# Kernel optimization log

Hardware: AMD Instinct MI355X
Metric: run time of the kernel (lower is better)

Reference implementation:

```python
import jax, jax.numpy as jnp
import numpy as np
from jax import lax

B, C, H, W = 2, 256, 64, 64
OUT_C = 256
D_QK = C // 16   # 16
D_V = C // 2     # 128
BN_EPS = 1e-5


def setup_inputs() -> dict:
    key = jax.random.key(0)
    ks = jax.random.split(key, 10)
    s = lambda fan: 1.0 / np.sqrt(fan)
    return {
        "input1": jax.random.normal(ks[0], (B, C, H, W), jnp.float32),
        "input2": jax.random.normal(ks[1], (B, C, H, W), jnp.float32),
        "Wq": jax.random.normal(ks[2], (D_QK, C), jnp.float32) * s(C),
        "bq": jnp.zeros((D_QK,), jnp.float32),
        "Wk": jax.random.normal(ks[3], (D_QK, C), jnp.float32) * s(C),
        "bk": jnp.zeros((D_QK,), jnp.float32),
        "Wv": jax.random.normal(ks[4], (D_V, C), jnp.float32) * s(C),
        "bv": jnp.zeros((D_V,), jnp.float32),
        "gamma": jnp.array(0.5, jnp.float32),  # nn.Parameter(zeros(1)); nonzero to exercise the path
        "Wcat": jax.random.normal(ks[5], (OUT_C, C, 3, 3), jnp.float32) * s(C * 9),
        "bn_gamma": jnp.ones((OUT_C,), jnp.float32),
        "bn_beta": jnp.zeros((OUT_C,), jnp.float32),
    }


def _conv1x1(x, Wt, b):
    # x: (B,C,H,W), Wt: (O,C) -> (B,O,H,W)
    return jnp.einsum('bchw,oc->bohw', x, Wt) + b[None, :, None, None]


def _branch(x_self, x_other, Wq, bq, Wk, bk, Wv, bv, gamma):
    N = H * W
    q = _conv1x1(x_self, Wq, bq).reshape(B, D_QK, N)   # q of self
    k = _conv1x1(x_other, Wk, bk).reshape(B, D_QK, N)  # k of other
    v = _conv1x1(x_self, Wv, bv).reshape(B, D_V, N)    # v of self
    # attn[b,n,m] = softmax_m( q[:,n] . k[:,m] / sqrt(d) )
    attn = jax.nn.softmax(jnp.einsum('bdn,bdm->bnm', q, k) / jnp.sqrt(jnp.float32(D_QK)), axis=-1)
    out = jnp.einsum('bcm,bnm->bcn', v, attn).reshape(B, D_V, H, W)  # v @ attn^T
    out = jnp.concatenate([out, x_self[:, :C // 2]], axis=1)  # (B,C,H,W)
    return gamma * out + x_self


def reference(input1, input2, Wq, bq, Wk, bk, Wv, bv, gamma, Wcat, bn_gamma, bn_beta):
    out1 = _branch(input1, input2, Wq, bq, Wk, bk, Wv, bv, gamma)
    out2 = _branch(input2, input1, Wq, bq, Wk, bk, Wv, bv, gamma)
    s = out1 + out2
    y = lax.conv_general_dilated(s, Wcat, (1, 1), 'SAME',
                                 dimension_numbers=('NCHW', 'OIHW', 'NCHW'))
    # BatchNorm (inference: running_mean=0, running_var=1)
    inv = 1.0 / jnp.sqrt(1.0 + BN_EPS)
    y = y * (bn_gamma * inv)[None, :, None, None] + bn_beta[None, :, None, None]
    feat_sum = jax.nn.relu(y)
    return (feat_sum, out1, out2)
```

## Files before the change

kernel.cpp:

```cpp
#include <hip/hip_runtime.h>

#define N_PIX 4096
#define CCH 256
#define DV 128

typedef __attribute__((ext_vector_type(8))) short bf16x8;
typedef __attribute__((ext_vector_type(4))) float f32x4;
typedef __attribute__((ext_vector_type(8))) short short8;

__device__ __forceinline__ short f2bf(float f) {
    unsigned u = __builtin_bit_cast(unsigned, f);
    u += 0x7fffu + ((u >> 16) & 1u);
    return (short)(u >> 16);
}

__device__ __forceinline__ float4 bf4_load(const short* p) {
    short4 s = *(const short4*)p;
    float4 f;
    f.x = __builtin_bit_cast(float, (unsigned)((unsigned short)s.x) << 16);
    f.y = __builtin_bit_cast(float, (unsigned)((unsigned short)s.y) << 16);
    f.z = __builtin_bit_cast(float, (unsigned)((unsigned short)s.z) << 16);
    f.w = __builtin_bit_cast(float, (unsigned)((unsigned short)s.w) << 16);
    return f;
}

__global__ __launch_bounds__(512) void qkv_kernel(
    const float* __restrict__ x1, const float* __restrict__ x2,
    const short* __restrict__ wqkv,
    const float* __restrict__ bq, const float* __restrict__ bk,
    const float* __restrict__ bv,
    short* __restrict__ qb, short* __restrict__ kb, short* __restrict__ vb)
{
    __shared__ short xT[64][68];

    const int tid = threadIdx.x;
    const int lane = tid & 63;
    const int w = tid >> 6;
    const int g = lane >> 4, l15 = lane & 15;
    const int n0 = blockIdx.x * 64;
    const int ib = blockIdx.y;
    const int i = ib >> 1, b = ib & 1;
    const float* x = (i == 0 ? x1 : x2) + (size_t)b * CCH * N_PIX;

    const int px2 = tid & 31, c4 = tid >> 5;
    const int rhalf = (w >> 2) * 80;

    f32x4 acc[5];
    #pragma unroll
    for (int jl = 0; jl < 5; ++jl) {
        int rbase = rhalf + jl * 16;
        float bias;
        if (rbase == 0)       bias = bq[l15];
        else if (rbase == 16) bias = bk[l15];
        else                  bias = bv[rbase - 32 + l15];
        acc[jl] = (f32x4){bias, bias, bias, bias};
    }

    float2 xr[4];
    {
        #pragma unroll
        for (int jj = 0; jj < 4; ++jj)
            xr[jj] = *(const float2*)&x[(size_t)(c4 * 4 + jj) * N_PIX + n0 + px2 * 2];
    }

    for (int ci = 0; ci < 4; ++ci) {
        __syncthreads();
        {
            short4 w0, w1;
            w0.x = f2bf(xr[0].x); w0.y = f2bf(xr[1].x); w0.z = f2bf(xr[2].x); w0.w = f2bf(xr[3].x);
            w1.x = f2bf(xr[0].y); w1.y = f2bf(xr[1].y); w1.z = f2bf(xr[2].y); w1.w = f2bf(xr[3].y);
            *(short4*)&xT[px2 * 2 + 0][c4 * 4] = w0;
            *(short4*)&xT[px2 * 2 + 1][c4 * 4] = w1;
        }
        __syncthreads();
        if (ci < 3) {
            #pragma unroll
            for (int jj = 0; jj < 4; ++jj)
                xr[jj] = *(const float2*)
                    &x[(size_t)((ci + 1) * 64 + c4 * 4 + jj) * N_PIX + n0 + px2 * 2];
        }
        bf16x8 a0 = *(const bf16x8*)&xT[(w & 3) * 16 + l15][g * 8];
        bf16x8 a1 = *(const bf16x8*)&xT[(w & 3) * 16 + l15][32 + g * 8];
        #pragma unroll
        for (int jl = 0; jl < 5; ++jl) {
            int rbase = rhalf + jl * 16;
            const short* wrow = wqkv + (size_t)(rbase + l15) * CCH + ci * 64;
            bf16x8 b0 = *(const bf16x8*)&wrow[g * 8];
            bf16x8 b1 = *(const bf16x8*)&wrow[32 + g * 8];
            acc[jl] = __builtin_amdgcn_mfma_f32_16x16x32_bf16(a0, b0, acc[jl], 0, 0, 0);
            acc[jl] = __builtin_amdgcn_mfma_f32_16x16x32_bf16(a1, b1, acc[jl], 0, 0, 0);
        }
    }

    const int px_base = n0 + (w & 3) * 16 + g * 4;
    #pragma unroll
    for (int jl = 0; jl < 5; ++jl) {
        int rbase = rhalf + jl * 16;
        if (rbase == 0) {
            #pragma unroll
            for (int rr = 0; rr < 4; ++rr)
                qb[((size_t)ib * N_PIX + px_base + rr) * 16 + l15] = f2bf(acc[jl][rr]);
        } else if (rbase == 16) {
            #pragma unroll
            for (int rr = 0; rr < 4; ++rr)
                kb[((size_t)ib * N_PIX + px_base + rr) * 16 + l15] = f2bf(acc[jl][rr]);
        } else {
            int c = rbase - 32 + l15;
            short4 s;
            s.x = f2bf(acc[jl][0]); s.y = f2bf(acc[jl][1]);
            s.z = f2bf(acc[jl][2]); s.w = f2bf(acc[jl][3]);
            *(short4*)&vb[((size_t)ib * DV + c) * N_PIX + px_base] = s;
        }
    }
}

__global__ __launch_bounds__(256, 4) void attn_kernel(
    const short* __restrict__ qg, const short* __restrict__ kg,
    const short* __restrict__ vg,
    float* __restrict__ out1, float* __restrict__ out2,
    short* __restrict__ featp, float* __restrict__ lpart)
{
    __shared__ short k_lds[64 * 24];
    __shared__ short p_lds[64 * 72];

    const int tid = threadIdx.x;
    const int lane = tid & 63;
    const int w = tid >> 6;
    const int gk = lane >> 4;
    const int l15 = lane & 15;

    const int B_ = blockIdx.x;
    const int pb = B_ & 3;
    const int mh = (B_ >> 2) % 3;
    const int nt = B_ / 12;
    const int n0 = nt * 64;
    const int br = pb >> 1, b = pb & 1;
    const int tstart = mh * 22;
    const int tend = (mh == 2) ? 64 : tstart + 22;

    const short* qp = qg + (size_t)pb * N_PIX * 16;
    const short* kp = kg + (size_t)((br ^ 1) * 2 + b) * N_PIX * 16;
    const short* vp = vg + (size_t)pb * DV * N_PIX;

    bf16x8 aq = {};
    if (lane < 32)
        aq = *(const bf16x8*)&qp[(size_t)(n0 + w * 16 + l15) * 16 + gk * 8];

    f32x4 acc[2][4];
    #pragma unroll
    for (int cc = 0; cc < 2; ++cc)
        #pragma unroll
        for (int nb = 0; nb < 4; ++nb) acc[cc][nb] = (f32x4){0.f, 0.f, 0.f, 0.f};
    float lsum[4] = {0.f, 0.f, 0.f, 0.f};

    const short* vbase = vp + (size_t)(w * 32 + l15) * N_PIX + gk * 8;
    const int krow = tid - 192;

    int4 vbuf0[4], vbuf1[4];
    int4 kr0 = {}, kr1 = {};

    {
        #pragma unroll
        for (int cc = 0; cc < 2; ++cc)
            #pragma unroll
            for (int m2 = 0; m2 < 2; ++m2)
                vbuf0[cc * 2 + m2] = *(const int4*)
                    &vbase[(size_t)cc * 16 * N_PIX + tstart * 64 + m2 * 32];
        if (tid >= 192) {
            kr0 = *(const int4*)&kp[(size_t)(tstart * 64 + krow) * 16];
            kr1 = *(const int4*)&kp[(size_t)(tstart * 64 + krow) * 16 + 8];
            *(int4*)&k_lds[krow * 24] = kr0;
            *(int4*)&k_lds[krow * 24 + 8] = kr1;
        }
        __syncthreads();
    }

    for (int t0 = tstart; t0 < tend; t0 += 2) {
        #pragma unroll
        for (int half = 0; half < 2; ++half) {
            const int t = t0 + half;
            int4* vcur = half ? vbuf1 : vbuf0;
            int4* vnxt = half ? vbuf0 : vbuf1;
            if (t + 1 < tend) {
                #pragma unroll
                for (int cc = 0; cc < 2; ++cc)
                    #pragma unroll
                    for (int m2 = 0; m2 < 2; ++m2)
                        vnxt[cc * 2 + m2] = *(const int4*)
                            &vbase[(size_t)cc * 16 * N_PIX + (t + 1) * 64 + m2 * 32];
                if (tid >= 192) {
                    kr0 = *(const int4*)&kp[(size_t)((t + 1) * 64 + krow) * 16];
                    kr1 = *(const int4*)&kp[(size_t)((t + 1) * 64 + krow) * 16 + 8];
                }
            }
            #pragma unroll
            for (int h = 0; h < 4; ++h) {
                bf16x8 bk_ = {};
                if (lane < 32)
                    bk_ = *(const bf16x8*)&k_lds[(h * 16 + l15) * 24 + gk * 8];
                f32x4 s = __builtin_amdgcn_mfma_f32_16x16x32_bf16(
                    aq, bk_, (f32x4){0.f, 0.f, 0.f, 0.f}, 0, 0, 0);
                #pragma unroll
                for (int rr = 0; rr < 4; ++rr) {
                    float e = __expf(s[rr] * 0.25f);
                    lsum[rr] += e;
                    unsigned u = __builtin_bit_cast(unsigned, e);
                    p_lds[(w * 16 + gk * 4 + rr) * 72 + h * 16 + l15] = (short)(u >> 16);
                }
            }
            __syncthreads();
            if (t + 1 < tend && tid >= 192) {
                *(int4*)&k_lds[krow * 24] = kr0;
                *(int4*)&k_lds[krow * 24 + 8] = kr1;
            }
            __builtin_amdgcn_s_setprio(1);
            #pragma unroll
            for (int m2 = 0; m2 < 2; ++m2) {
                #pragma unroll
                for (int nb = 0; nb < 4; ++nb) {
                    bf16x8 bp = *(const bf16x8*)&p_lds[(nb * 16 + l15) * 72 + m2 * 32 + gk * 8];
                    #pragma unroll
                    for (int cc = 0; cc < 2; ++cc) {
                        bf16x8 av = __builtin_bit_cast(bf16x8, vcur[cc * 2 + m2]);
                        acc[cc][nb] = __builtin_amdgcn_mfma_f32_16x16x32_bf16(
                            av, bp, acc[cc][nb], 0, 0, 0);
                    }
                }
            }
            __builtin_amdgcn_s_setprio(0);
            __syncthreads();
        }
    }

    #pragma unroll
    for (int rr = 0; rr < 4; ++rr) {
        float v = lsum[rr];
        v += __shfl_xor(v, 1); v += __shfl_xor(v, 2);
        v += __shfl_xor(v, 4); v += __shfl_xor(v, 8);
        lsum[rr] = v;
    }
    if (l15 == 0) {
        #pragma unroll
        for (int rr = 0; rr < 4; ++rr)
            lpart[(size_t)(pb * 3 + mh) * N_PIX + n0 + w * 16 + gk * 4 + rr] = lsum[rr];
    }

    if (mh == 0) {
        float* Od = (br ? out2 : out1) + (size_t)b * CCH * N_PIX;
        #pragma unroll
        for (int cc = 0; cc < 2; ++cc)
            #pragma unroll
            for (int nb = 0; nb < 4; ++nb)
                #pragma unroll
                for (int rr = 0; rr < 4; ++rr) {
                    int c = w * 32 + cc * 16 + gk * 4 + rr;
                    Od[(size_t)c * N_PIX + n0 + nb * 16 + l15] = acc[cc][nb][rr];
                }
    } else {
        short* Ps = featp + (size_t)(pb * 2 + (mh - 1)) * (64 * 128 * 64)
                          + (size_t)nt * (128 * 64);
        #pragma unroll
        for (int chalf = 0; chalf < 2; ++chalf) {
            if ((w >> 1) == chalf) {
                int crel_base = (w & 1) * 32;
                #pragma unroll
                for (int cc = 0; cc < 2; ++cc)
                    #pragma unroll
                    for (int nb = 0; nb < 4; ++nb)
                        #pragma unroll
                        for (int rr = 0; rr < 4; ++rr) {
                            int crel = crel_base + cc * 16 + gk * 4 + rr;
                            p_lds[crel * 66 + nb * 16 + l15] = f2bf(acc[cc][nb][rr]);
                        }
            }
            __syncthreads();
            for (int idx = tid; idx < 512; idx += 256) {
                int cr = idx >> 3, seg = idx & 7;
                int4 v = *(const int4*)&p_lds[cr * 66 + seg * 8];
                *(int4*)&Ps[(size_t)(chalf * 64 + cr) * 64 + seg * 8] = v;
            }
            __syncthreads();
        }
    }
}

__global__ __launch_bounds__(256) void merge_kernel(
    const float* __restrict__ x1, const float* __restrict__ x2,
    const short* __restrict__ featp, const float* __restrict__ lpart,
    const float* __restrict__ gamma_p,
    float* __restrict__ out1, float* __restrict__ out2,
    short* __restrict__ s_t)
{
    __shared__ short st[32 * 264];
    __shared__ float rls[2][32];
    const int tid = threadIdx.x;
    const int px0 = blockIdx.x * 32;
    const int b = blockIdx.y;
    const int nt = blockIdx.x >> 1;
    const int q32 = (blockIdx.x & 1) * 32;
    const float* xa_ = x1 + (size_t)b * CCH * N_PIX;
    const float* xb_ = x2 + (size_t)b * CCH * N_PIX;
    float* o1 = out1 + (size_t)b * CCH * N_PIX;
    float* o2 = out2 + (size_t)b * CCH * N_PIX;
    const short* T10 = featp + (size_t)(b * 2 + 0) * (64 * 128 * 64) + (size_t)nt * (128 * 64);
    const short* T11 = featp + (size_t)(b * 2 + 1) * (64 * 128 * 64) + (size_t)nt * (128 * 64);
    const short* T20 = featp + (size_t)((2 + b) * 2 + 0) * (64 * 128 * 64) + (size_t)nt * (128 * 64);
    const short* T21 = featp + (size_t)((2 + b) * 2 + 1) * (64 * 128 * 64) + (size_t)nt * (128 * 64);

    if (tid < 64) {
        int h = tid >> 5, j = tid & 31;
        int pbh = h ? (2 + b) : b;
        float l = lpart[(size_t)(pbh * 3 + 0) * N_PIX + px0 + j]
                + lpart[(size_t)(pbh * 3 + 1) * N_PIX + px0 + j]
                + lpart[(size_t)(pbh * 3 + 2) * N_PIX + px0 + j];
        rls[h][j] = 1.0f / l;
    }
    __syncthreads();
    const float gmm = gamma_p[0];

    for (int idx = tid; idx < 2048; idx += 256) {
        int c = idx >> 3, p4 = idx & 7;
        size_t off = (size_t)c * N_PIX + px0 + p4 * 4;
        float4 va = *(const float4*)&xa_[off];
        float4 vb2 = *(const float4*)&xb_[off];
        float4 r1, r2;
        if (c < 128) {
            int toff = c * 64 + q32 + p4 * 4;
            float4 pa = *(const float4*)&o1[off];
            float4 pc = *(const float4*)&o2[off];
            float4 a1 = bf4_load(&T10[toff]);
            float4 a2 = bf4_load(&T11[toff]);
            float4 c1 = bf4_load(&T20[toff]);
            float4 c2 = bf4_load(&T21[toff]);
            r1.x = gmm * (pa.x + a1.x + a2.x) * rls[0][p4 * 4 + 0] + va.x;
            r1.y = gmm * (pa.y + a1.y + a2.y) * rls[0][p4 * 4 + 1] + va.y;
            r1.z = gmm * (pa.z + a1.z + a2.z) * rls[0][p4 * 4 + 2] + va.z;
            r1.w = gmm * (pa.w + a1.w + a2.w) * rls[0][p4 * 4 + 3] + va.w;
            r2.x = gmm * (pc.x + c1.x + c2.x) * rls[1][p4 * 4 + 0] + vb2.x;
            r2.y = gmm * (pc.y + c1.y + c2.y) * rls[1][p4 * 4 + 1] + vb2.y;
            r2.z = gmm * (pc.z + c1.z + c2.z) * rls[1][p4 * 4 + 2] + vb2.z;
            r2.w = gmm * (pc.w + c1.w + c2.w) * rls[1][p4 * 4 + 3] + vb2.w;
        } else {
            size_t offl = (size_t)(c - 128) * N_PIX + px0 + p4 * 4;
            float4 val = *(const float4*)&xa_[offl];
            float4 vbl = *(const float4*)&xb_[offl];
            r1.x = gmm * val.x + va.x; r1.y = gmm * val.y + va.y;
            r1.z = gmm * val.z + va.z; r1.w = gmm * val.w + va.w;
            r2.x = gmm * vbl.x + vb2.x; r2.y = gmm * vbl.y + vb2.y;
            r2.z = gmm * vbl.z + vb2.z; r2.w = gmm * vbl.w + vb2.w;
        }
        *(float4*)&o1[off] = r1;
        *(float4*)&o2[off] = r2;
        st[(p4 * 4 + 0) * 264 + c] = f2bf(r1.x + r2.x);
        st[(p4 * 4 + 1) * 264 + c] = f2bf(r1.y + r2.y);
        st[(p4 * 4 + 2) * 264 + c] = f2bf(r1.z + r2.z);
        st[(p4 * 4 + 3) * 264 + c] = f2bf(r1.w + r2.w);
    }
    __syncthreads();
    for (int idx = tid; idx < 1024; idx += 256) {
        int px = idx >> 5, seg = idx & 31;
        int4 v = *(const int4*)&st[px * 264 + seg * 8];
        *(int4*)&s_t[((size_t)b * N_PIX + px0 + px) * CCH + seg * 8] = v;
    }
}

__global__ __launch_bounds__(256) void prep_w(
    const float* __restrict__ Wcat,
    const float* __restrict__ Wq, const float* __restrict__ Wk,
    const float* __restrict__ Wv,
    short* __restrict__ wfmt, short* __restrict__ wqkv)
{
    if (blockIdx.x < 288) {
        int idx = blockIdx.x * 256 + threadIdx.x;
        int lane = idx & 63;
        int ocg = (idx >> 6) & 15;
        int chunk = (idx >> 10) & 7;
        int tap = idx >> 13;
        int oc = ocg * 16 + (lane & 15);
        int ic0 = chunk * 32 + (lane >> 4) * 8;
        short8 v;
        #pragma unroll
        for (int j = 0; j < 8; ++j)
            v[j] = f2bf(Wcat[((size_t)oc * CCH + ic0 + j) * 9 + tap]);
        *(short8*)&wfmt[(size_t)idx * 8] = v;
    } else {
        int idx = (blockIdx.x - 288) * 1024 + threadIdx.x * 4;
        int r = idx >> 8, c = idx & 255;
        const float* src;
        if (r < 16)      src = Wq + (size_t)r * CCH + c;
        else if (r < 32) src = Wk + (size_t)(r - 16) * CCH + c;
        else             src = Wv + (size_t)(r - 32) * CCH + c;
        float4 f = *(const float4*)src;
        short4 s;
        s.x = f2bf(f.x); s.y = f2bf(f.y); s.z = f2bf(f.z); s.w = f2bf(f.w);
        *(short4*)&wqkv[idx] = s;
    }
}

__global__ __launch_bounds__(256, 2) void conv_mfma(
    const short* __restrict__ s_t, const short* __restrict__ wfmt,
    const float* __restrict__ bn_gamma, const float* __restrict__ bn_beta,
    float* __restrict__ feat)
{
    __shared__ short s_lds[198 * 40];
    const int tid = threadIdx.x;
    const int lane = tid & 63;
    const int wv = tid >> 6;
    const int g = lane >> 4, l15 = lane & 15;

    const int bx = blockIdx.x;
    const int oc_t = bx & 3;
    const int pt = bx >> 2;
    const int b = pt >> 6;
    const int h0 = pt & 63;

    f32x4 acc[4] = {};

    const short* sbase = s_t + (size_t)b * N_PIX * CCH;
    const short* wf = wfmt + ((size_t)(oc_t * 4) * 64 + lane) * 8;

    for (int ci = 0; ci < 8; ++ci) {
        const int ic0 = ci * 32;
        __syncthreads();
        for (int idx = tid; idx < 792; idx += 256) {
            int seg = idx & 3, pos = idx >> 2;
            int row = pos / 66, wi = pos - row * 66;
            int hr = h0 - 1 + row, w = wi - 1;
            int4 val = {0, 0, 0, 0};
            if (hr >= 0 && hr < 64 && (unsigned)w < 64u)
                val = *(const int4*)&sbase[((size_t)(hr * 64 + w)) * CCH + ic0 + seg * 8];
            *(int4*)&s_lds[pos * 40 + seg * 8] = val;
        }
        __syncthreads();

        const short* wfc = wf + (size_t)ci * 8192;
        bf16x8 a0[4], a1[4];
        #pragma unroll
        for (int j = 0; j < 4; ++j) a0[j] = *(const bf16x8*)&wfc[j * 512];

        for (int tap = 0; tap < 9; ++tap) {
            bf16x8* ac = (tap & 1) ? a1 : a0;
            bf16x8* an = (tap & 1) ? a0 : a1;
            if (tap < 8) {
                const short* wfn = wfc + (size_t)(tap + 1) * 65536;
                #pragma unroll
                for (int j = 0; j < 4; ++j) an[j] = *(const bf16x8*)&wfn[j * 512];
            }
            int ky = (tap >= 6) ? 2 : (tap >= 3 ? 1 : 0);
            int kx = tap - ky * 3;
            bf16x8 bb = *(const bf16x8*)
                &s_lds[(ky * 66 + wv * 16 + l15 + kx) * 40 + g * 8];
            #pragma unroll
            for (int j = 0; j < 4; ++j)
                acc[j] = __builtin_amdgcn_mfma_f32_16x16x32_bf16(
                    ac[j], bb, acc[j], 0, 0, 0);
        }
    }

    const float inv = rsqrtf(1.0f + 1e-5f);
    const int wcol = wv * 16 + l15;
    #pragma unroll
    for (int j = 0; j < 4; ++j) {
        #pragma unroll
        for (int r = 0; r < 4; ++r) {
            int oc = oc_t * 64 + j * 16 + g * 4 + r;
            float y = acc[j][r] * (bn_gamma[oc] * inv) + bn_beta[oc];
            feat[((size_t)b * CCH + oc) * N_PIX + h0 * 64 + wcol] = fmaxf(y, 0.f);
        }
    }
}

extern "C" void kernel_launch(void* const* d_in, const int* in_sizes, int n_in,
                              void* d_out, int out_size, void* d_ws, size_t ws_size,
                              hipStream_t stream) {
    const float* x1    = (const float*)d_in[0];
    const float* x2    = (const float*)d_in[1];
    const float* Wq    = (const float*)d_in[2];
    const float* bq    = (const float*)d_in[3];
    const float* Wk    = (const float*)d_in[4];
    const float* bk    = (const float*)d_in[5];
    const float* Wv    = (const float*)d_in[6];
    const float* bv    = (const float*)d_in[7];
    const float* gamma = (const float*)d_in[8];
    const float* Wcat  = (const float*)d_in[9];
    const float* bng   = (const float*)d_in[10];
    const float* bnb   = (const float*)d_in[11];

    float* out  = (float*)d_out;
    float* feat = out;
    float* out1 = out + 2097152;
    float* out2 = out + 4194304;

    short* ws   = (short*)d_ws;
    short* qb   = ws;
    short* kb   = ws + 262144;
    short* vb   = ws + 524288;
    short* s_t  = ws + 2621440;
    short* wfmt = ws + 4718592;
    float* lp   = (float*)(ws + 5308416);
    short* wqkv = s_t;

    prep_w<<<328, 256, 0, stream>>>(Wcat, Wq, Wk, Wv, wfmt, wqkv);
    qkv_kernel<<<dim3(64, 4), 512, 0, stream>>>(x1, x2, wqkv, bq, bk, bv, qb, kb, vb);
    attn_kernel<<<768, 256, 0, stream>>>(qb, kb, vb, out1, out2, (short*)feat, lp);
    merge_kernel<<<dim3(128, 2), 256, 0, stream>>>(x1, x2, (const short*)feat, lp, gamma, out1, out2, s_t);
    conv_mfma<<<512, 256, 0, stream>>>(s_t, wfmt, bng, bnb, feat);
}
```

Measured before the change: 107.1 us.

## Load K fragments directly to registers and double-buffer P tile to drop barrier

The attention kernel no longer stages K through shared memory. Each lane now loads its MFMA K fragments straight from global memory into double-buffered registers. The P tile in LDS is double-buffered by half-step, which removes the second __syncthreads per inner step; the LDS row pitch also changes from 72 to 68. The extra register buffers lower the launch-bounds occupancy hint from 4 to 3 blocks per CU, which may reduce latency hiding.

```diff
diff --git a/kernel.cpp b/kernel.cpp
--- a/kernel.cpp
+++ b/kernel.cpp
@@ -114,14 +114,13 @@
     }
 }
 
-__global__ __launch_bounds__(256, 4) void attn_kernel(
+__global__ __launch_bounds__(256, 3) void attn_kernel(
     const short* __restrict__ qg, const short* __restrict__ kg,
     const short* __restrict__ vg,
     float* __restrict__ out1, float* __restrict__ out2,
     short* __restrict__ featp, float* __restrict__ lpart)
 {
-    __shared__ short k_lds[64 * 24];
-    __shared__ short p_lds[64 * 72];
+    __shared__ short p_lds[2][64 * 68];
 
     const int tid = threadIdx.x;
     const int lane = tid & 63;
@@ -154,10 +153,10 @@
     float lsum[4] = {0.f, 0.f, 0.f, 0.f};
 
     const short* vbase = vp + (size_t)(w * 32 + l15) * N_PIX + gk * 8;
-    const int krow = tid - 192;
+    const short* kfrag = kp + (size_t)l15 * 16 + gk * 8;
 
     int4 vbuf0[4], vbuf1[4];
-    int4 kr0 = {}, kr1 = {};
+    int4 kbuf0[4] = {}, kbuf1[4] = {};
 
     {
         #pragma unroll
@@ -166,13 +165,11 @@
             for (int m2 = 0; m2 < 2; ++m2)
                 vbuf0[cc * 2 + m2] = *(const int4*)
                     &vbase[(size_t)cc * 16 * N_PIX + tstart * 64 + m2 * 32];
-        if (tid >= 192) {
-            kr0 = *(const int4*)&kp[(size_t)(tstart * 64 + krow) * 16];
-            kr1 = *(const int4*)&kp[(size_t)(tstart * 64 + krow) * 16 + 8];
-            *(int4*)&k_lds[krow * 24] = kr0;
-            *(int4*)&k_lds[krow * 24 + 8] = kr1;
-        }
-        __syncthreads();
+        if (lane < 32) {
+            #pragma unroll
+            for (int h = 0; h < 4; ++h)
+                kbuf0[h] = *(const int4*)&kfrag[(size_t)(tstart * 64 + h * 16) * 16];
+        }
     }
 
     for (int t0 = tstart; t0 < tend; t0 += 2) {
@@ -181,6 +178,9 @@
             const int t = t0 + half;
             int4* vcur = half ? vbuf1 : vbuf0;
             int4* vnxt = half ? vbuf0 : vbuf1;
+            int4* kcur = half ? kbuf1 : kbuf0;
+            int4* knxt = half ? kbuf0 : kbuf1;
+            short* pcur = &p_lds[half][0];
             if (t + 1 < tend) {
                 #pragma unroll
                 for (int cc = 0; cc < 2; ++cc)
@@ -188,16 +188,15 @@
                     for (int m2 = 0; m2 < 2; ++m2)
                         vnxt[cc * 2 + m2] = *(const int4*)
                             &vbase[(size_t)cc * 16 * N_PIX + (t + 1) * 64 + m2 * 32];
-                if (tid >= 192) {
-                    kr0 = *(const int4*)&kp[(size_t)((t + 1) * 64 + krow) * 16];
-                    kr1 = *(const int4*)&kp[(size_t)((t + 1) * 64 + krow) * 16 + 8];
+                if (lane < 32) {
+                    #pragma unroll
+                    for (int h = 0; h < 4; ++h)
+                        knxt[h] = *(const int4*)&kfrag[(size_t)((t + 1) * 64 + h * 16) * 16];
                 }
             }
             #pragma unroll
             for (int h = 0; h < 4; ++h) {
-                bf16x8 bk_ = {};
-                if (lane < 32)
-                    bk_ = *(const bf16x8*)&k_lds[(h * 16 + l15) * 24 + gk * 8];
+                bf16x8 bk_ = __builtin_bit_cast(bf16x8, kcur[h]);
                 f32x4 s = __builtin_amdgcn_mfma_f32_16x16x32_bf16(
                     aq, bk_, (f32x4){0.f, 0.f, 0.f, 0.f}, 0, 0, 0);
                 #pragma unroll
@@ -205,20 +204,16 @@
                     float e = __expf(s[rr] * 0.25f);
                     lsum[rr] += e;
                     unsigned u = __builtin_bit_cast(unsigned, e);
-                    p_lds[(w * 16 + gk * 4 + rr) * 72 + h * 16 + l15] = (short)(u >> 16);
+                    pcur[(w * 16 + gk * 4 + rr) * 68 + h * 16 + l15] = (short)(u >> 16);
                 }
             }
             __syncthreads();
-            if (t + 1 < tend && tid >= 192) {
-                *(int4*)&k_lds[krow * 24] = kr0;
-                *(int4*)&k_lds[krow * 24 + 8] = kr1;
-            }
             __builtin_amdgcn_s_setprio(1);
             #pragma unroll
             for (int m2 = 0; m2 < 2; ++m2) {
                 #pragma unroll
                 for (int nb = 0; nb < 4; ++nb) {
-                    bf16x8 bp = *(const bf16x8*)&p_lds[(nb * 16 + l15) * 72 + m2 * 32 + gk * 8];
+                    bf16x8 bp = *(const bf16x8*)&pcur[(nb * 16 + l15) * 68 + m2 * 32 + gk * 8];
                     #pragma unroll
                     for (int cc = 0; cc < 2; ++cc) {
                         bf16x8 av = __builtin_bit_cast(bf16x8, vcur[cc * 2 + m2]);
@@ -228,7 +223,6 @@
                 }
             }
             __builtin_amdgcn_s_setprio(0);
-            __syncthreads();
         }
     }
 
@@ -257,6 +251,8 @@
                     Od[(size_t)c * N_PIX + n0 + nb * 16 + l15] = acc[cc][nb][rr];
                 }
     } else {
+        __syncthreads();
+        short* pf = &p_lds[0][0];
         short* Ps = featp + (size_t)(pb * 2 + (mh - 1)) * (64 * 128 * 64)
                           + (size_t)nt * (128 * 64);
         #pragma unroll
@@ -270,13 +266,13 @@
                         #pragma unroll
                         for (int rr = 0; rr < 4; ++rr) {
                             int crel = crel_base + cc * 16 + gk * 4 + rr;
-                            p_lds[crel * 66 + nb * 16 + l15] = f2bf(acc[cc][nb][rr]);
+                            pf[crel * 66 + nb * 16 + l15] = f2bf(acc[cc][nb][rr]);
                         }
             }
             __syncthreads();
             for (int idx = tid; idx < 512; idx += 256) {
                 int cr = idx >> 3, seg = idx & 7;
-                int4 v = *(const int4*)&p_lds[cr * 66 + seg * 8];
+                int4 v = *(const int4*)&pf[cr * 66 + seg * 8];
                 *(int4*)&Ps[(size_t)(chalf * 64 + cr) * 64 + seg * 8] = v;
             }
             __syncthreads();
```

Result: slower. 142.1 us (+32.7%).

## Retile PV MFMA warps to 64ch x 32pix and single-buffer V loads

Applied to the files above, without the earlier changes.

Changes the per-warp output tile of the P·V product from 32 channels × 64 pixels to 64 channels × 32 pixels, so each warp reads half as many P fragments from LDS but holds twice as many V fragments. The double-buffered V register prefetch is replaced by a single buffer refilled after the MFMA block of each tile, and the unroll-by-two loop becomes a plain per-tile loop. This keeps the register count roughly the same but gives up the overlap of the V global loads with compute, so V load latency may be exposed before the next barrier.

```diff
diff --git a/kernel.cpp b/kernel.cpp
--- a/kernel.cpp
+++ b/kernel.cpp
@@ -146,25 +146,28 @@
     if (lane < 32)
         aq = *(const bf16x8*)&qp[(size_t)(n0 + w * 16 + l15) * 16 + gk * 8];
 
-    f32x4 acc[2][4];
+    const int ch = w & 1;
+    const int nh = w >> 1;
+
+    f32x4 acc[4][2];
     #pragma unroll
-    for (int cc = 0; cc < 2; ++cc)
-        #pragma unroll
-        for (int nb = 0; nb < 4; ++nb) acc[cc][nb] = (f32x4){0.f, 0.f, 0.f, 0.f};
+    for (int cc = 0; cc < 4; ++cc)
+        #pragma unroll
+        for (int nb = 0; nb < 2; ++nb) acc[cc][nb] = (f32x4){0.f, 0.f, 0.f, 0.f};
     float lsum[4] = {0.f, 0.f, 0.f, 0.f};
 
-    const short* vbase = vp + (size_t)(w * 32 + l15) * N_PIX + gk * 8;
+    const short* vbase = vp + (size_t)(ch * 64 + l15) * N_PIX + gk * 8;
     const int krow = tid - 192;
 
-    int4 vbuf0[4], vbuf1[4];
+    int4 vbuf[8];
     int4 kr0 = {}, kr1 = {};
 
     {
         #pragma unroll
-        for (int cc = 0; cc < 2; ++cc)
+        for (int cc = 0; cc < 4; ++cc)
             #pragma unroll
             for (int m2 = 0; m2 < 2; ++m2)
-                vbuf0[cc * 2 + m2] = *(const int4*)
+                vbuf[cc * 2 + m2] = *(const int4*)
                     &vbase[(size_t)cc * 16 * N_PIX + tstart * 64 + m2 * 32];
         if (tid >= 192) {
             kr0 = *(const int4*)&kp[(size_t)(tstart * 64 + krow) * 16];
@@ -175,61 +178,56 @@
         __syncthreads();
     }
 
-    for (int t0 = tstart; t0 < tend; t0 += 2) {
-        #pragma unroll
-        for (int half = 0; half < 2; ++half) {
-            const int t = t0 + half;
-            int4* vcur = half ? vbuf1 : vbuf0;
-            int4* vnxt = half ? vbuf0 : vbuf1;
-            if (t + 1 < tend) {
+    for (int t = tstart; t < tend; ++t) {
+        if (t + 1 < tend && tid >= 192) {
+            kr0 = *(const int4*)&kp[(size_t)((t + 1) * 64 + krow) * 16];
+            kr1 = *(const int4*)&kp[(size_t)((t + 1) * 64 + krow) * 16 + 8];
+        }
+        #pragma unroll
+        for (int h = 0; h < 4; ++h) {
+            bf16x8 bk_ = {};
+            if (lane < 32)
+                bk_ = *(const bf16x8*)&k_lds[(h * 16 + l15) * 24 + gk * 8];
+            f32x4 s = __builtin_amdgcn_mfma_f32_16x16x32_bf16(
+                aq, bk_, (f32x4){0.f, 0.f, 0.f, 0.f}, 0, 0, 0);
+            #pragma unroll
+            for (int rr = 0; rr < 4; ++rr) {
+                float e = __expf(s[rr] * 0.25f);
+                lsum[rr] += e;
+                unsigned u = __builtin_bit_cast(unsigned, e);
+                p_lds[(w * 16 + gk * 4 + rr) * 72 + h * 16 + l15] = (short)(u >> 16);
+            }
+        }
+        __syncthreads();
+        if (t + 1 < tend && tid >= 192) {
+            *(int4*)&k_lds[krow * 24] = kr0;
+            *(int4*)&k_lds[krow * 24 + 8] = kr1;
+        }
+        __builtin_amdgcn_s_setprio(1);
+        #pragma unroll
+        for (int m2 = 0; m2 < 2; ++m2) {
+            #pragma unroll
+            for (int nb = 0; nb < 2; ++nb) {
+                bf16x8 bp = *(const bf16x8*)
+                    &p_lds[(nh * 32 + nb * 16 + l15) * 72 + m2 * 32 + gk * 8];
                 #pragma unroll
-                for (int cc = 0; cc < 2; ++cc)
-                    #pragma unroll
-                    for (int m2 = 0; m2 < 2; ++m2)
-                        vnxt[cc * 2 + m2] = *(const int4*)
-                            &vbase[(size_t)cc * 16 * N_PIX + (t + 1) * 64 + m2 * 32];
-                if (tid >= 192) {
-                    kr0 = *(const int4*)&kp[(size_t)((t + 1) * 64 + krow) * 16];
-                    kr1 = *(const int4*)&kp[(size_t)((t + 1) * 64 + krow) * 16 + 8];
+                for (int cc = 0; cc < 4; ++cc) {
+                    bf16x8 av = __builtin_bit_cast(bf16x8, vbuf[cc * 2 + m2]);
+                    acc[cc][nb] = __builtin_amdgcn_mfma_f32_16x16x32_bf16(
+                        av, bp, acc[cc][nb], 0, 0, 0);
                 }
             }
-            #pragma unroll
-            for (int h = 0; h < 4; ++h) {
-                bf16x8 bk_ = {};
-                if (lane < 32)
-                    bk_ = *(const bf16x8*)&k_lds[(h * 16 + l15) * 24 + gk * 8];
-                f32x4 s = __builtin_amdgcn_mfma_f32_16x16x32_bf16(
-                    aq, bk_, (f32x4){0.f, 0.f, 0.f, 0.f}, 0, 0, 0);
+        }
+        __builtin_amdgcn_s_setprio(0);
+        if (t + 1 < tend) {
+            #pragma unroll
+            for (int cc = 0; cc < 4; ++cc)
                 #pragma unroll
-                for (int rr = 0; rr < 4; ++rr) {
-                    float e = __expf(s[rr] * 0.25f);
-                    lsum[rr] += e;
-                    unsigned u = __builtin_bit_cast(unsigned, e);
-                    p_lds[(w * 16 + gk * 4 + rr) * 72 + h * 16 + l15] = (short)(u >> 16);
-                }
-            }
-            __syncthreads();
-            if (t + 1 < tend && tid >= 192) {
-                *(int4*)&k_lds[krow * 24] = kr0;
-                *(int4*)&k_lds[krow * 24 + 8] = kr1;
-            }
-            __builtin_amdgcn_s_setprio(1);
-            #pragma unroll
-            for (int m2 = 0; m2 < 2; ++m2) {
-                #pragma unroll
-                for (int nb = 0; nb < 4; ++nb) {
-                    bf16x8 bp = *(const bf16x8*)&p_lds[(nb * 16 + l15) * 72 + m2 * 32 + gk * 8];
-                    #pragma unroll
-                    for (int cc = 0; cc < 2; ++cc) {
-                        bf16x8 av = __builtin_bit_cast(bf16x8, vcur[cc * 2 + m2]);
-                        acc[cc][nb] = __builtin_amdgcn_mfma_f32_16x16x32_bf16(
-                            av, bp, acc[cc][nb], 0, 0, 0);
-                    }
-                }
-            }
-            __builtin_amdgcn_s_setprio(0);
-            __syncthreads();
-        }
+                for (int m2 = 0; m2 < 2; ++m2)
+                    vbuf[cc * 2 + m2] = *(const int4*)
+                        &vbase[(size_t)cc * 16 * N_PIX + (t + 1) * 64 + m2 * 32];
+        }
+        __syncthreads();
     }
 
     #pragma unroll
@@ -248,29 +246,30 @@
     if (mh == 0) {
         float* Od = (br ? out2 : out1) + (size_t)b * CCH * N_PIX;
         #pragma unroll
-        for (int cc = 0; cc < 2; ++cc)
-            #pragma unroll
-            for (int nb = 0; nb < 4; ++nb)
+        for (int cc = 0; cc < 4; ++cc)
+            #pragma unroll
+            for (int nb = 0; nb < 2; ++nb)
                 #pragma unroll
                 for (int rr = 0; rr < 4; ++rr) {
-                    int c = w * 32 + cc * 16 + gk * 4 + rr;
-                    Od[(size_t)c * N_PIX + n0 + nb * 16 + l15] = acc[cc][nb][rr];
+                    int c = ch * 64 + cc * 16 + gk * 4 + rr;
+                    int n = n0 + nh * 32 + nb * 16 + l15;
+                    Od[(size_t)c * N_PIX + n] = acc[cc][nb][rr];
                 }
     } else {
         short* Ps = featp + (size_t)(pb * 2 + (mh - 1)) * (64 * 128 * 64)
                           + (size_t)nt * (128 * 64);
         #pragma unroll
         for (int chalf = 0; chalf < 2; ++chalf) {
-            if ((w >> 1) == chalf) {
-                int crel_base = (w & 1) * 32;
+            if (ch == chalf) {
                 #pragma unroll
-                for (int cc = 0; cc < 2; ++cc)
+                for (int cc = 0; cc < 4; ++cc)
                     #pragma unroll
-                    for (int nb = 0; nb < 4; ++nb)
+                    for (int nb = 0; nb < 2; ++nb)
                         #pragma unroll
                         for (int rr = 0; rr < 4; ++rr) {
-                            int crel = crel_base + cc * 16 + gk * 4 + rr;
-                            p_lds[crel * 66 + nb * 16 + l15] = f2bf(acc[cc][nb][rr]);
+                            int crel = cc * 16 + gk * 4 + rr;
+                            int ncol = nh * 32 + nb * 16 + l15;
+                            p_lds[crel * 66 + ncol] = f2bf(acc[cc][nb][rr]);
                         }
             }
             __syncthreads();
```

New measurement: 133.4 us. 24.6% more time.
